# Performance work log

Measured on AMD Instinct MI355X. Metric: run time of the kernel, lower is better.

## Reference

```python
import jax, jax.numpy as jnp
import numpy as np

D = 768; NH = 12; HD = D // NH; L = 12; NC = 27; PATCH = 16; MLP = 3072; PROJ = 512
IMG = 224; GRID = IMG // PATCH; HW = GRID * GRID; S = NC + HW
NEG = -1e9

def _ln(x, w, b):
    m = jnp.mean(x, -1, keepdims=True)
    v = jnp.mean(jnp.square(x - m), -1, keepdims=True)
    return (x - m) * jax.lax.rsqrt(v + 1e-5) * w + b

def _quick_gelu(x):
    return x * jax.nn.sigmoid(1.702 * x)

def _build_mask(attn_obj_masks, dtype):
    # CRIS block mask: cls<->cls blocked except self; cls->patch allowed only for
    # patches of that class; patch->cls blocked; patch->patch fully allowed.
    B = attn_obj_masks.shape[0]
    oh = jax.nn.one_hot(attn_obj_masks, NC, dtype=dtype)              # [B, HW, NC]
    T11 = jnp.broadcast_to(1.0 - jnp.eye(NC, dtype=dtype), (B, NC, NC))
    M13 = 1.0 - jnp.swapaxes(oh, 1, 2)                                # [B, NC, HW]
    top = jnp.concatenate([T11, M13], axis=2)
    bot = jnp.concatenate([jnp.ones((B, HW, NC), dtype), jnp.zeros((B, HW, HW), dtype)], axis=2)
    Mb = jnp.concatenate([top, bot], axis=1)                          # [B, S, S]
    return jnp.where(Mb == 1.0, jnp.asarray(NEG, dtype), jnp.asarray(0.0, dtype))

def reference(img, sents, attn_obj_masks, obj_masks, cls_tokens, patch_w, patch_b, pos_embed,
              ln1_w, ln1_b, qkv_w, qkv_b, out_w, out_b, ln2_w, ln2_b,
              mlp_w1, mlp_b1, mlp_w2, mlp_b2, ln_post_w, ln_post_b, proj):
    B = img.shape[0]
    sents = sents / jnp.linalg.norm(sents, axis=-1, keepdims=True)    # encode_text output, L2 normed
    mask = _build_mask(attn_obj_masks, img.dtype)                     # [B, S, S]
    # patch embedding (conv stride 16) -> [B, HW, D]
    p = jax.lax.conv_general_dilated(img, patch_w, (PATCH, PATCH), 'VALID',
                                     dimension_numbers=('NCHW', 'OIHW', 'NCHW'))
    p = p.reshape(B, D, HW).transpose(0, 2, 1) + patch_b
    x = jnp.concatenate([jnp.broadcast_to(cls_tokens, (B, NC, D)), p], axis=1) + pos_embed
    scale = 1.0 / np.sqrt(HD).astype(np.float32)
    def block(x, prm):
        l1w, l1b, qw, qb, ow, ob, l2w, l2b, w1, b1, w2, b2 = prm
        h = _ln(x, l1w, l1b)
        qkv = h @ qw + qb
        q, k, v = jnp.split(qkv, 3, axis=-1)
        q = q.reshape(B, S, NH, HD).transpose(0, 2, 1, 3)
        k = k.reshape(B, S, NH, HD).transpose(0, 2, 1, 3)
        v = v.reshape(B, S, NH, HD).transpose(0, 2, 1, 3)
        scores = jnp.einsum('bhqd,bhkd->bhqk', q, k) * scale + mask[:, None]
        a = jax.nn.softmax(scores, axis=-1)
        o = jnp.einsum('bhqk,bhkd->bhqd', a, v).transpose(0, 2, 1, 3).reshape(B, S, D)
        x = x + o @ ow + ob
        h = _ln(x, l2w, l2b)
        x = x + _quick_gelu(h @ w1 + b1) @ w2 + b2
        return x, None
    x, _ = jax.lax.scan(block, x, (ln1_w, ln1_b, qkv_w, qkv_b, out_w, out_b,
                                   ln2_w, ln2_b, mlp_w1, mlp_b1, mlp_w2, mlp_b2))
    tokens = _ln(x, ln_post_w, ln_post_b) @ proj                      # [B, S, PROJ]
    obj = tokens[:, :NC]
    obj = obj / jnp.linalg.norm(obj, axis=-1, keepdims=True)
    pred_id = jnp.einsum('bnd,bd->bn', obj, sents)                    # [B, NC]
    # per-class scatter loop == gather of pred_id by per-pixel class id
    pred = jnp.take_along_axis(pred_id, obj_masks.reshape(B, -1), axis=1).reshape(obj_masks.shape)
    return pred                                                       # [B, 224, 224]

def setup_inputs():
    B = 16; std = 0.02
    ks = jax.random.split(jax.random.key(0), 16)
    f = jax.random.normal
    return {
        'img': f(ks[0], (B, 3, IMG, IMG), jnp.float32),
        'sents': f(ks[1], (B, PROJ), jnp.float32),
        'attn_obj_masks': jax.random.randint(ks[2], (B, HW), 0, NC, jnp.int32),
        'obj_masks': jax.random.randint(ks[3], (B, IMG, IMG), 0, NC, jnp.int32),
        'cls_tokens': f(ks[4], (1, NC, D)) * std,
        'patch_w': f(ks[5], (D, 3, PATCH, PATCH)) * std,
        'patch_b': jnp.zeros((D,)),
        'pos_embed': f(ks[6], (S, D)) * std,
        'ln1_w': jnp.ones((L, D)), 'ln1_b': jnp.zeros((L, D)),
        'qkv_w': f(ks[7], (L, D, 3 * D)) * std, 'qkv_b': jnp.zeros((L, 3 * D)),
        'out_w': f(ks[8], (L, D, D)) * std, 'out_b': jnp.zeros((L, D)),
        'ln2_w': jnp.ones((L, D)), 'ln2_b': jnp.zeros((L, D)),
        'mlp_w1': f(ks[9], (L, D, MLP)) * std, 'mlp_b1': jnp.zeros((L, MLP)),
        'mlp_w2': f(ks[10], (L, MLP, D)) * std, 'mlp_b2': jnp.zeros((L, D)),
        'ln_post_w': jnp.ones((D,)), 'ln_post_b': jnp.zeros((D,)),
        'proj': f(ks[11], (D, PROJ)) * std,
    }
```

## Files before the change

### kernel.cpp

```cpp
#include <hip/hip_runtime.h>

#define DEV __device__ __forceinline__

typedef short bf16x8 __attribute__((ext_vector_type(8)));
typedef float f32x4 __attribute__((ext_vector_type(4)));
typedef int vi4 __attribute__((ext_vector_type(4)));
typedef unsigned short u16;
typedef short short4v __attribute__((ext_vector_type(4)));

#define NEGV -1000000000.0f

DEV u16 f2bf(float f) {
  union { float f; unsigned u; } v; v.f = f;
  unsigned r = v.u + 0x7FFFu + ((v.u >> 16) & 1u);
  return (u16)(r >> 16);
}

DEV bf16x8 ld_bf8(const u16* p) {
  vi4 v = *(const vi4*)p;
  return __builtin_bit_cast(bf16x8, v);
}

DEV void gload_lds16(const u16* g, vi4* l) {
  __builtin_amdgcn_global_load_lds((const __attribute__((address_space(1))) void*)g,
                                   (__attribute__((address_space(3))) void*)l, 16, 0, 0);
}

template<int BN, int MODE, bool GELU, int KS>
__global__ __launch_bounds__(256) void gemm_bt(
    const u16* __restrict__ A, const u16* __restrict__ Bt,
    const float* __restrict__ bias,
    float* __restrict__ Cf, u16* __restrict__ Cb,
    int M, int N, int K, const float* __restrict__ pos, long pstride)
{
  constexpr int FJ = BN / 32;
  constexpr int LTOT = 4 + FJ;
  __shared__ vi4 As[2][1024];
  __shared__ vi4 Bs[2][BN * 8];

  int gx = gridDim.x, gy = gridDim.y;
  int nwg = gx * gy * (int)gridDim.z;
  int orig = blockIdx.x + gx * (blockIdx.y + gy * blockIdx.z);
  int qq = nwg >> 3, rr = nwg & 7;
  int xcd = orig & 7, off = orig >> 3;
  int id = (xcd < rr) ? xcd * (qq + 1) + off : rr * (qq + 1) + (xcd - rr) * qq + off;
  int bx = id % gx, rest = id / gx, by = rest % gy, bz = rest / gy;

  int tid = threadIdx.x, lane = tid & 63, wid = tid >> 6;
  int wm = wid >> 1, wn = wid & 1;
  int m0 = by * 128, n0 = bx * BN;
  int kBeg = (K / KS) * bz;
  int nT = (K / KS) >> 6;
  f32x4 acc[4][FJ] = {};

  auto STAGE = [&](int buf, int kk) {
    #pragma unroll
    for (int r = 0; r < 4; ++r) {
      int flat = r * 256 + tid;
      int row = flat >> 3, c = flat & 7;
      int cs = c ^ (row & 7);
      gload_lds16(A + (long)(m0 + row) * K + kk + cs * 8, &As[buf][r * 256 + wid * 64]);
    }
    #pragma unroll
    for (int r = 0; r < FJ; ++r) {
      int flat = r * 256 + tid;
      int row = flat >> 3, c = flat & 7;
      int cs = c ^ (row & 7);
      gload_lds16(Bt + (long)(n0 + row) * K + kk + cs * 8, &Bs[buf][r * 256 + wid * 64]);
    }
  };

  STAGE(0, kBeg);
  int cur = 0;
  for (int t = 0; t < nT; ++t) {
    if (t + 1 < nT) {
      STAGE(cur ^ 1, kBeg + (t + 1) * 64);
      asm volatile("s_waitcnt vmcnt(%0)" :: "i"(LTOT) : "memory");
    } else {
      asm volatile("s_waitcnt vmcnt(0)" ::: "memory");
    }
    __builtin_amdgcn_s_barrier();
    int cg = lane >> 4, l15 = lane & 15;
    #pragma unroll
    for (int ks = 0; ks < 2; ++ks) {
      bf16x8 af[4], bfr[FJ];
      #pragma unroll
      for (int i = 0; i < 4; ++i) {
        int ra = wm * 64 + i * 16 + l15;
        af[i] = __builtin_bit_cast(bf16x8, As[cur][ra * 8 + ((ks * 4 + cg) ^ (ra & 7))]);
      }
      #pragma unroll
      for (int j = 0; j < FJ; ++j) {
        int rb = wn * (BN / 2) + j * 16 + l15;
        bfr[j] = __builtin_bit_cast(bf16x8, Bs[cur][rb * 8 + ((ks * 4 + cg) ^ (rb & 7))]);
      }
      #pragma unroll
      for (int i = 0; i < 4; ++i)
        #pragma unroll
        for (int j = 0; j < FJ; ++j)
          acc[i][j] = __builtin_amdgcn_mfma_f32_16x16x32_bf16(af[i], bfr[j], acc[i][j], 0, 0, 0);
    }
    __builtin_amdgcn_s_barrier();
    cur ^= 1;
  }

  int cg = lane >> 4, l15 = lane & 15;
  float* Cfz = (MODE == 2 && KS > 1) ? Cf + (long)bz * pstride : Cf;
  #pragma unroll
  for (int i = 0; i < 4; ++i) {
    #pragma unroll
    for (int j = 0; j < FJ; ++j) {
      int col = n0 + wn * (BN / 2) + j * 16 + l15;
      float bv = bias ? bias[col] : 0.f;
      #pragma unroll
      for (int r = 0; r < 4; ++r) {
        int row = m0 + wm * 64 + i * 16 + cg * 4 + r;
        if (row < M) {
          float v = acc[i][j][r];
          if (KS == 1 || bz == 0) v += bv;
          if (GELU) v = v / (1.f + __expf(-1.702f * v));
          if (MODE == 0) Cb[(long)row * N + col] = f2bf(v);
          else if (MODE == 2) Cfz[(long)row * N + col] = v;
          else {
            int hw = row % 196;
            int xr = (row / 196) * 223 + 27 + hw;
            Cf[(long)xr * 768 + col] = v + pos[(27 + hw) * 768 + col];
          }
        }
      }
    }
  }
}

__global__ __launch_bounds__(256) void attn_kernel(
    const u16* __restrict__ QKV, const int* __restrict__ aom, u16* __restrict__ O)
{
  __shared__ vi4 Kl[224 * 8];
  __shared__ vi4 Vt[64 * 28];
  __shared__ vi4 Pl[4][16 * 28];
  __shared__ int ml[196];
  int tid = threadIdx.x, lane = tid & 63, wid = tid >> 6;
  int qg = blockIdx.x, h = blockIdx.y, b = blockIdx.z;
  long rowbase = (long)b * 223;
  #pragma unroll
  for (int it = 0; it < 7; ++it) {
    int flat = it * 256 + tid;
    int s = flat >> 3, c = flat & 7;
    int cs = c ^ (s & 7);
    gload_lds16(QKV + (rowbase + s) * 2304 + 768 + h * 64 + cs * 8, &Kl[it * 256 + wid * 64]);
  }
  u16* vt16 = (u16*)Vt;
  #pragma unroll
  for (int it = 0; it < 7; ++it) {
    int flat = it * 256 + tid;
    int s = flat >> 3, c = flat & 7;
    vi4 v = {0, 0, 0, 0};
    if (s < 223) v = *(const vi4*)(QKV + (rowbase + s) * 2304 + 1536 + h * 64 + c * 8);
    union { vi4 v4; u16 hx[8]; } uu; uu.v4 = v;
    int cs = s >> 3;
    #pragma unroll
    for (int j = 0; j < 8; ++j) {
      int d = c * 8 + j;
      vt16[d * 224 + (cs ^ ((d >> 1) & 3)) * 8 + (s & 7)] = uu.hx[j];
    }
  }
  for (int i = tid; i < 196; i += 256) ml[i] = aom[b * 196 + i];
  __syncthreads();

  int colk = lane & 15, cg = lane >> 4;
  #pragma unroll
  for (int rep = 0; rep < 2; ++rep) {
    int fo = wid * 2 + rep;
    if (fo >= 7) break;
    int qf = qg * 7 + fo;
    int q0 = qf * 16;
    int arow = q0 + colk; if (arow > 222) arow = 222;
    const u16* qb = QKV + (rowbase + arow) * 2304 + h * 64;
    bf16x8 aq0 = ld_bf8(qb + cg * 8);
    bf16x8 aq1 = ld_bf8(qb + 32 + cg * 8);

    f32x4 sc[14];
    #pragma unroll
    for (int kf = 0; kf < 14; ++kf) {
      int key = kf * 16 + colk;
      f32x4 a = {0.f, 0.f, 0.f, 0.f};
      bf16x8 bk0 = __builtin_bit_cast(bf16x8, Kl[key * 8 + (cg ^ (key & 7))]);
      bf16x8 bk1 = __builtin_bit_cast(bf16x8, Kl[key * 8 + ((4 + cg) ^ (key & 7))]);
      a = __builtin_amdgcn_mfma_f32_16x16x32_bf16(aq0, bk0, a, 0, 0, 0);
      a = __builtin_amdgcn_mfma_f32_16x16x32_bf16(aq1, bk1, a, 0, 0, 0);
      sc[kf] = a;
    }
    #pragma unroll
    for (int r = 0; r < 4; ++r) {
      int q = q0 + cg * 4 + r;
      float mx = -3.4e38f;
      #pragma unroll
      for (int kf = 0; kf < 14; ++kf) {
        int key = kf * 16 + colk;
        float mval;
        if (key >= 223) mval = NEGV;
        else if (q >= 27) mval = (key < 27) ? NEGV : 0.f;
        else if (key < 27) mval = (key == q) ? 0.f : NEGV;
        else mval = (ml[key - 27] == q) ? 0.f : NEGV;
        float s = sc[kf][r] * 0.125f + mval;
        sc[kf][r] = s;
        mx = fmaxf(mx, s);
      }
      #pragma unroll
      for (int d = 1; d < 16; d <<= 1) mx = fmaxf(mx, __shfl_xor(mx, d));
      float sum = 0.f;
      #pragma unroll
      for (int kf = 0; kf < 14; ++kf) {
        float e = __expf(sc[kf][r] - mx);
        sc[kf][r] = e; sum += e;
      }
      #pragma unroll
      for (int d = 1; d < 16; d <<= 1) sum += __shfl_xor(sum, d);
      float inv = 1.f / sum;
      #pragma unroll
      for (int kf = 0; kf < 14; ++kf) sc[kf][r] *= inv;
    }
    u16* pw = (u16*)Pl[wid];
    #pragma unroll
    for (int kf = 0; kf < 14; ++kf) {
      int key = kf * 16 + colk;
      int ck = key >> 3;
      #pragma unroll
      for (int r = 0; r < 4; ++r) {
        int prow = cg * 4 + r;
        pw[prow * 224 + (ck ^ ((prow >> 1) & 3)) * 8 + (key & 7)] = f2bf(sc[kf][r]);
      }
    }
    f32x4 oacc[4] = {};
    #pragma unroll
    for (int ks = 0; ks < 7; ++ks) {
      bf16x8 pa = __builtin_bit_cast(bf16x8, Pl[wid][colk * 28 + ((ks * 4 + cg) ^ ((colk >> 1) & 3))]);
      #pragma unroll
      for (int nf = 0; nf < 4; ++nf) {
        int d = nf * 16 + colk;
        bf16x8 bv = __builtin_bit_cast(bf16x8, Vt[d * 28 + ((ks * 4 + cg) ^ ((d >> 1) & 3))]);
        oacc[nf] = __builtin_amdgcn_mfma_f32_16x16x32_bf16(pa, bv, oacc[nf], 0, 0, 0);
      }
    }
    #pragma unroll
    for (int nf = 0; nf < 4; ++nf) {
      int d = h * 64 + nf * 16 + colk;
      #pragma unroll
      for (int r = 0; r < 4; ++r) {
        int q = q0 + cg * 4 + r;
        if (q < 223) O[(rowbase + q) * 768 + d] = f2bf(oacc[nf][r]);
      }
    }
  }
}

template<int NADD, bool MAP27, bool WRITEX>
__global__ __launch_bounds__(256) void ln_kernel(
    const float* __restrict__ X, const float* __restrict__ P, long ps,
    float* __restrict__ Xout, u16* __restrict__ Hb,
    const float* __restrict__ w, const float* __restrict__ bb, int nrows)
{
  int row = blockIdx.x * 4 + (threadIdx.x >> 6);
  if (row >= nrows) return;
  int xr = MAP27 ? (row / 27) * 223 + (row % 27) : row;
  int l = threadIdx.x & 63;
  const float4* xp = (const float4*)(X + (long)xr * 768);
  float4 a = xp[l], c = xp[l + 64], d = xp[l + 128];
  if (NADD == 2) {
    const float4* p0 = (const float4*)(P + (long)xr * 768);
    const float4* p1 = (const float4*)(P + ps + (long)xr * 768);
    float4 u0 = p0[l], u1 = p0[l + 64], u2 = p0[l + 128];
    float4 v0 = p1[l], v1 = p1[l + 64], v2 = p1[l + 128];
    a.x += u0.x + v0.x; a.y += u0.y + v0.y; a.z += u0.z + v0.z; a.w += u0.w + v0.w;
    c.x += u1.x + v1.x; c.y += u1.y + v1.y; c.z += u1.z + v1.z; c.w += u1.w + v1.w;
    d.x += u2.x + v2.x; d.y += u2.y + v2.y; d.z += u2.z + v2.z; d.w += u2.w + v2.w;
  }
  if (WRITEX) {
    float4* xo = (float4*)(Xout + (long)xr * 768);
    xo[l] = a; xo[l + 64] = c; xo[l + 128] = d;
  }
  float s = a.x + a.y + a.z + a.w + c.x + c.y + c.z + c.w + d.x + d.y + d.z + d.w;
  #pragma unroll
  for (int t = 1; t < 64; t <<= 1) s += __shfl_xor(s, t);
  float mean = s * (1.f / 768.f);
  a.x -= mean; a.y -= mean; a.z -= mean; a.w -= mean;
  c.x -= mean; c.y -= mean; c.z -= mean; c.w -= mean;
  d.x -= mean; d.y -= mean; d.z -= mean; d.w -= mean;
  float q = a.x*a.x + a.y*a.y + a.z*a.z + a.w*a.w
          + c.x*c.x + c.y*c.y + c.z*c.z + c.w*c.w
          + d.x*d.x + d.y*d.y + d.z*d.z + d.w*d.w;
  #pragma unroll
  for (int t = 1; t < 64; t <<= 1) q += __shfl_xor(q, t);
  float rs = rsqrtf(q * (1.f / 768.f) + 1e-5f);
  const float4* wp = (const float4*)w;
  const float4* bp = (const float4*)bb;
  u16* out = Hb + (long)row * 768;
  float4 w0 = wp[l], w1 = wp[l + 64], w2 = wp[l + 128];
  float4 b0 = bp[l], b1 = bp[l + 64], b2 = bp[l + 128];
  short4v o;
  o[0] = (short)f2bf(a.x * rs * w0.x + b0.x); o[1] = (short)f2bf(a.y * rs * w0.y + b0.y);
  o[2] = (short)f2bf(a.z * rs * w0.z + b0.z); o[3] = (short)f2bf(a.w * rs * w0.w + b0.w);
  *(short4v*)(out + l * 4) = o;
  o[0] = (short)f2bf(c.x * rs * w1.x + b1.x); o[1] = (short)f2bf(c.y * rs * w1.y + b1.y);
  o[2] = (short)f2bf(c.z * rs * w1.z + b1.z); o[3] = (short)f2bf(c.w * rs * w1.w + b1.w);
  *(short4v*)(out + 256 + l * 4) = o;
  o[0] = (short)f2bf(d.x * rs * w2.x + b2.x); o[1] = (short)f2bf(d.y * rs * w2.y + b2.y);
  o[2] = (short)f2bf(d.z * rs * w2.z + b2.z); o[3] = (short)f2bf(d.w * rs * w2.w + b2.w);
  *(short4v*)(out + 512 + l * 4) = o;
}

__global__ __launch_bounds__(256) void transpose_w(
    const float* __restrict__ W, u16* __restrict__ WT, int K, int N, long sW, long sT)
{
  __shared__ float t[64][65];
  int z = blockIdx.z;
  W += (long)z * sW; WT += (long)z * sT;
  int n0 = blockIdx.x * 64, k0 = blockIdx.y * 64;
  #pragma unroll
  for (int i = 0; i < 4; ++i) {
    int flat = i * 256 + threadIdx.x;
    int r = flat >> 4, c = (flat & 15) * 4;
    float4 v = *(const float4*)(W + (long)(k0 + r) * N + n0 + c);
    t[r][c] = v.x; t[r][c + 1] = v.y; t[r][c + 2] = v.z; t[r][c + 3] = v.w;
  }
  __syncthreads();
  #pragma unroll
  for (int i = 0; i < 8; ++i) {
    int flat = i * 256 + threadIdx.x;
    int rn = flat >> 5, ck = (flat & 31) * 2;
    unsigned val = (unsigned)f2bf(t[ck][rn]) | ((unsigned)f2bf(t[ck + 1][rn]) << 16);
    *(unsigned*)(WT + (long)(n0 + rn) * K + k0 + ck) = val;
  }
}

__global__ void convert_bf16(const float* __restrict__ src, u16* __restrict__ dst, int n) {
  int i = blockIdx.x * 256 + threadIdx.x;
  if (i < n) dst[i] = f2bf(src[i]);
}

__global__ __launch_bounds__(192) void patch_extract(const float* __restrict__ img, u16* __restrict__ Xp) {
  int row = blockIdx.x;
  int t = threadIdx.x;
  int pair = t >> 2, part = t & 3;
  int cch = pair >> 4, kh = pair & 15;
  int b = row / 196, hw = row % 196, gh = hw / 14, gw = hw % 14;
  float4 v = *(const float4*)(img + ((long)(b * 3 + cch) * 224 + gh * 16 + kh) * 224 + gw * 16 + part * 4);
  short4v o;
  o[0] = (short)f2bf(v.x); o[1] = (short)f2bf(v.y); o[2] = (short)f2bf(v.z); o[3] = (short)f2bf(v.w);
  *(short4v*)(Xp + (long)row * 768 + pair * 16 + part * 4) = o;
}

__global__ void cls_pos_fill(const float* __restrict__ cls, const float* __restrict__ pos, float* __restrict__ x) {
  int i = blockIdx.x * 256 + threadIdx.x;
  if (i >= 16 * 27 * 768) return;
  int d = i % 768, t = i / 768, b = t / 27, s = t % 27;
  x[((long)b * 223 + s) * 768 + d] = cls[s * 768 + d] + pos[s * 768 + d];
}

__global__ __launch_bounds__(256) void sents_norm(const float* __restrict__ s, float* __restrict__ sn) {
  __shared__ float sb[4];
  int b = blockIdx.x, t = threadIdx.x;
  float v0 = s[b * 512 + t], v1 = s[b * 512 + t + 256];
  float q = v0 * v0 + v1 * v1;
  #pragma unroll
  for (int d = 1; d < 64; d <<= 1) q += __shfl_xor(q, d);
  if ((t & 63) == 0) sb[t >> 6] = q;
  __syncthreads();
  float inv = rsqrtf(sb[0] + sb[1] + sb[2] + sb[3]);
  sn[b * 512 + t] = v0 * inv;
  sn[b * 512 + t + 256] = v1 * inv;
}

__global__ __launch_bounds__(256) void obj_dot(const float* __restrict__ obj, const float* __restrict__ sn, float* __restrict__ pid) {
  __shared__ float sb[8];
  int r = blockIdx.x, t = threadIdx.x, b = r / 27;
  float v0 = obj[(long)r * 512 + t], v1 = obj[(long)r * 512 + t + 256];
  float w0 = sn[b * 512 + t], w1 = sn[b * 512 + t + 256];
  float q = v0 * v0 + v1 * v1;
  float dt = v0 * w0 + v1 * w1;
  #pragma unroll
  for (int d = 1; d < 64; d <<= 1) { q += __shfl_xor(q, d); dt += __shfl_xor(dt, d); }
  if ((t & 63) == 0) { sb[t >> 6] = q; sb[4 + (t >> 6)] = dt; }
  __syncthreads();
  if (t == 0) pid[r] = (sb[4] + sb[5] + sb[6] + sb[7]) * rsqrtf(sb[0] + sb[1] + sb[2] + sb[3]);
}

__global__ void gather_pred(const int* __restrict__ om, const float* __restrict__ pid, float* __restrict__ out) {
  int i = blockIdx.x * 256 + threadIdx.x;
  if (i >= 16 * 224 * 224) return;
  int b = i / (224 * 224);
  out[i] = pid[b * 27 + om[i]];
}

extern "C" void kernel_launch(void* const* d_in, const int* in_sizes, int n_in,
                              void* d_out, int out_size, void* d_ws, size_t ws_size,
                              hipStream_t stream) {
  const float* img     = (const float*)d_in[0];
  const float* sents   = (const float*)d_in[1];
  const int*   aom     = (const int*)d_in[2];
  const int*   omask   = (const int*)d_in[3];
  const float* cls     = (const float*)d_in[4];
  const float* patch_w = (const float*)d_in[5];
  const float* patch_b = (const float*)d_in[6];
  const float* pos     = (const float*)d_in[7];
  const float* ln1w    = (const float*)d_in[8];
  const float* ln1b    = (const float*)d_in[9];
  const float* qkvw    = (const float*)d_in[10];
  const float* qkvb    = (const float*)d_in[11];
  const float* outw    = (const float*)d_in[12];
  const float* outb    = (const float*)d_in[13];
  const float* ln2w    = (const float*)d_in[14];
  const float* ln2b    = (const float*)d_in[15];
  const float* m1w     = (const float*)d_in[16];
  const float* m1b     = (const float*)d_in[17];
  const float* m2w     = (const float*)d_in[18];
  const float* m2b     = (const float*)d_in[19];
  const float* lnpw    = (const float*)d_in[20];
  const float* lnpb    = (const float*)d_in[21];
  const float* projw   = (const float*)d_in[22];

  char* p = (char*)d_ws;
  auto alloc = [&](size_t bytes) { char* r = p; p += (bytes + 255) & ~(size_t)255; return r; };
  const long PS = 3584l * 768;
  float* x   = (float*)alloc(3568ul * 768 * 4);
  u16* H     = (u16*)alloc(3584ul * 768 * 2);
  u16* QKV   = (u16*)alloc(3584ul * 2304 * 2);
  u16* Obuf  = (u16*)alloc(3584ul * 768 * 2);
  u16* G     = (u16*)alloc(3584ul * 3072 * 2);
  float* Y   = (float*)alloc((size_t)PS * 2 * 4);
  float* Mp  = (float*)alloc((size_t)PS * 2 * 4);
  u16* PWc   = (u16*)alloc(768ul * 768 * 2);
  u16* PrT   = (u16*)alloc(512ul * 768 * 2);
  float* obj = (float*)alloc(432ul * 512 * 4);
  float* sn  = (float*)alloc(16ul * 512 * 4);
  float* pid = (float*)alloc(432ul * 4);

  const size_t wlayer = (2304ul * 768 + 768ul * 768 + 3072ul * 768 + 768ul * 3072) * 2;
  size_t used = (size_t)(p - (char*)d_ws);
  int nw = (ws_size >= used + 12 * wlayer + 65536) ? 12 : 1;
  const long sQ = 2304l * 768, sO = 768l * 768, s1 = 768l * 3072, s2 = 3072l * 768;
  u16* WqT = (u16*)alloc((size_t)sQ * 2 * nw);
  u16* WoT = (u16*)alloc((size_t)sO * 2 * nw);
  u16* W1T = (u16*)alloc((size_t)s1 * 2 * nw);
  u16* W2T = (u16*)alloc((size_t)s2 * 2 * nw);

  convert_bf16<<<2304, 256, 0, stream>>>(patch_w, PWc, 768 * 768);
  transpose_w<<<dim3(8, 12, 1), 256, 0, stream>>>(projw, PrT, 768, 512, 0, 0);
  if (nw == 12) {
    transpose_w<<<dim3(36, 12, 12), 256, 0, stream>>>(qkvw, WqT, 768, 2304, sQ, sQ);
    transpose_w<<<dim3(12, 12, 12), 256, 0, stream>>>(outw, WoT, 768, 768, sO, sO);
    transpose_w<<<dim3(48, 12, 12), 256, 0, stream>>>(m1w, W1T, 768, 3072, s1, s1);
    transpose_w<<<dim3(12, 48, 12), 256, 0, stream>>>(m2w, W2T, 3072, 768, s2, s2);
  }
  patch_extract<<<3136, 192, 0, stream>>>(img, H);
  cls_pos_fill<<<1296, 256, 0, stream>>>(cls, pos, x);
  gemm_bt<64, 3, false, 1><<<dim3(12, 25), 256, 0, stream>>>(H, PWc, patch_b, x, nullptr, 3136, 768, 768, pos, 0);

  for (int l = 0; l < 12; ++l) {
    u16 *wq, *wo, *w1, *w2;
    if (nw == 12) { wq = WqT + (long)l * sQ; wo = WoT + (long)l * sO; w1 = W1T + (long)l * s1; w2 = W2T + (long)l * s2; }
    else {
      wq = WqT; wo = WoT; w1 = W1T; w2 = W2T;
      transpose_w<<<dim3(36, 12, 1), 256, 0, stream>>>(qkvw + (long)l * sQ, wq, 768, 2304, 0, 0);
      transpose_w<<<dim3(12, 12, 1), 256, 0, stream>>>(outw + (long)l * sO, wo, 768, 768, 0, 0);
      transpose_w<<<dim3(48, 12, 1), 256, 0, stream>>>(m1w + (long)l * s1, w1, 768, 3072, 0, 0);
      transpose_w<<<dim3(12, 48, 1), 256, 0, stream>>>(m2w + (long)l * s2, w2, 3072, 768, 0, 0);
    }
    if (l == 0)
      ln_kernel<0, false, false><<<892, 256, 0, stream>>>(x, nullptr, 0, nullptr, H, ln1w, ln1b, 3568);
    else
      ln_kernel<2, false, true><<<892, 256, 0, stream>>>(x, Mp, PS, x, H, ln1w + l * 768, ln1b + l * 768, 3568);
    gemm_bt<128, 0, false, 1><<<dim3(18, 28), 256, 0, stream>>>(H, wq, qkvb + l * 2304, nullptr, QKV, 3568, 2304, 768, nullptr, 0);
    attn_kernel<<<dim3(2, 12, 16), 256, 0, stream>>>(QKV, aom, Obuf);
    gemm_bt<64, 2, false, 2><<<dim3(12, 28, 2), 256, 0, stream>>>(Obuf, wo, outb + l * 768, Y, nullptr, 3568, 768, 768, nullptr, PS);
    ln_kernel<2, false, true><<<892, 256, 0, stream>>>(x, Y, PS, x, H, ln2w + l * 768, ln2b + l * 768, 3568);
    gemm_bt<128, 0, true, 1><<<dim3(24, 28), 256, 0, stream>>>(H, w1, m1b + l * 3072, nullptr, G, 3568, 3072, 768, nullptr, 0);
    gemm_bt<64, 2, false, 2><<<dim3(12, 28, 2), 256, 0, stream>>>(G, w2, m2b + l * 768, Mp, nullptr, 3568, 768, 3072, nullptr, PS);
  }

  ln_kernel<2, true, false><<<108, 256, 0, stream>>>(x, Mp, PS, nullptr, H, lnpw, lnpb, 432);
  gemm_bt<64, 2, false, 1><<<dim3(8, 4), 256, 0, stream>>>(H, PrT, nullptr, obj, nullptr, 432, 512, 768, nullptr, 0);
  sents_norm<<<16, 256, 0, stream>>>(sents, sn);
  obj_dot<<<432, 256, 0, stream>>>(obj, sn, pid);
  gather_pred<<<3136, 256, 0, stream>>>(omask, pid, (float*)d_out);
}
```

Measured before the change: 2.377 ms.

## Use transposed LDS reads for V and keep softmax probabilities in registers

The attention kernel now loads V directly into LDS with async global_load_lds in a swizzled row-major layout and reads it with ds_read_b64_tr_b16 transpose loads. This replaces the scalar per-element transpose scatter into LDS. It also swaps the QK^T MFMA operands so each lane holds one query's scores, which cuts the softmax reductions to two shuffles. Probabilities move between lanes by shuffles instead of a round trip through LDS. The cost is extra shuffles, an explicit lgkmcnt wait, and reliance on the gfx950 transpose-load instruction and its lane mapping being right.

```diff
diff --git a/kernel.cpp b/kernel.cpp
--- a/kernel.cpp
+++ b/kernel.cpp
@@ -5,6 +5,7 @@
 typedef short bf16x8 __attribute__((ext_vector_type(8)));
 typedef float f32x4 __attribute__((ext_vector_type(4)));
 typedef int vi4 __attribute__((ext_vector_type(4)));
+typedef unsigned uint2v __attribute__((ext_vector_type(2)));
 typedef unsigned short u16;
 typedef short short4v __attribute__((ext_vector_type(4)));
 
@@ -24,6 +25,16 @@
 DEV void gload_lds16(const u16* g, vi4* l) {
   __builtin_amdgcn_global_load_lds((const __attribute__((address_space(1))) void*)g,
                                    (__attribute__((address_space(3))) void*)l, 16, 0, 0);
+}
+
+DEV unsigned lds_off(const void* p) {
+  return (unsigned)(unsigned long long)(const __attribute__((address_space(3))) void*)p;
+}
+
+DEV uint2v ds_tr16(unsigned byteaddr) {
+  uint2v r;
+  asm volatile("ds_read_b64_tr_b16 %0, %1" : "=v"(r) : "v"(byteaddr));
+  return r;
 }
 
 template<int BN, int MODE, bool GELU, int KS>
@@ -136,8 +147,7 @@
     const u16* __restrict__ QKV, const int* __restrict__ aom, u16* __restrict__ O)
 {
   __shared__ vi4 Kl[224 * 8];
-  __shared__ vi4 Vt[64 * 28];
-  __shared__ vi4 Pl[4][16 * 28];
+  __shared__ vi4 Vl[224 * 8];
   __shared__ int ml[196];
   int tid = threadIdx.x, lane = tid & 63, wid = tid >> 6;
   int qg = blockIdx.x, h = blockIdx.y, b = blockIdx.z;
@@ -149,32 +159,27 @@
     int cs = c ^ (s & 7);
     gload_lds16(QKV + (rowbase + s) * 2304 + 768 + h * 64 + cs * 8, &Kl[it * 256 + wid * 64]);
   }
-  u16* vt16 = (u16*)Vt;
   #pragma unroll
   for (int it = 0; it < 7; ++it) {
-    int flat = it * 256 + tid;
-    int s = flat >> 3, c = flat & 7;
-    vi4 v = {0, 0, 0, 0};
-    if (s < 223) v = *(const vi4*)(QKV + (rowbase + s) * 2304 + 1536 + h * 64 + c * 8);
-    union { vi4 v4; u16 hx[8]; } uu; uu.v4 = v;
-    int cs = s >> 3;
-    #pragma unroll
-    for (int j = 0; j < 8; ++j) {
-      int d = c * 8 + j;
-      vt16[d * 224 + (cs ^ ((d >> 1) & 3)) * 8 + (s & 7)] = uu.hx[j];
-    }
+    int u = it * 256 + tid;
+    int slin = u >> 3, inner = u & 7;
+    int sk = slin >> 2, sdp = slin & 3;
+    int s = sk * 4 + (inner >> 1);
+    int c = ((sdp ^ (sk & 3)) << 1) | (inner & 1);
+    gload_lds16(QKV + (rowbase + s) * 2304 + 1536 + h * 64 + c * 8, &Vl[it * 256 + wid * 64]);
   }
   for (int i = tid; i < 196; i += 256) ml[i] = aom[b * 196 + i];
   __syncthreads();
 
-  int colk = lane & 15, cg = lane >> 4;
+  int l15 = lane & 15, cg = lane >> 4;
+  unsigned vbase = lds_off(Vl);
   #pragma unroll
   for (int rep = 0; rep < 2; ++rep) {
     int fo = wid * 2 + rep;
     if (fo >= 7) break;
     int qf = qg * 7 + fo;
     int q0 = qf * 16;
-    int arow = q0 + colk; if (arow > 222) arow = 222;
+    int arow = q0 + l15; if (arow > 222) arow = 222;
     const u16* qb = QKV + (rowbase + arow) * 2304 + h * 64;
     bf16x8 aq0 = ld_bf8(qb + cg * 8);
     bf16x8 aq1 = ld_bf8(qb + 32 + cg * 8);
@@ -182,73 +187,84 @@
     f32x4 sc[14];
     #pragma unroll
     for (int kf = 0; kf < 14; ++kf) {
-      int key = kf * 16 + colk;
+      int key = kf * 16 + l15;
       f32x4 a = {0.f, 0.f, 0.f, 0.f};
       bf16x8 bk0 = __builtin_bit_cast(bf16x8, Kl[key * 8 + (cg ^ (key & 7))]);
       bf16x8 bk1 = __builtin_bit_cast(bf16x8, Kl[key * 8 + ((4 + cg) ^ (key & 7))]);
-      a = __builtin_amdgcn_mfma_f32_16x16x32_bf16(aq0, bk0, a, 0, 0, 0);
-      a = __builtin_amdgcn_mfma_f32_16x16x32_bf16(aq1, bk1, a, 0, 0, 0);
+      a = __builtin_amdgcn_mfma_f32_16x16x32_bf16(bk0, aq0, a, 0, 0, 0);
+      a = __builtin_amdgcn_mfma_f32_16x16x32_bf16(bk1, aq1, a, 0, 0, 0);
       sc[kf] = a;
     }
-    #pragma unroll
-    for (int r = 0; r < 4; ++r) {
-      int q = q0 + cg * 4 + r;
-      float mx = -3.4e38f;
-      #pragma unroll
-      for (int kf = 0; kf < 14; ++kf) {
-        int key = kf * 16 + colk;
+    int q = q0 + l15;
+    float mx = -3.4e38f;
+    #pragma unroll
+    for (int kf = 0; kf < 14; ++kf) {
+      #pragma unroll
+      for (int r = 0; r < 4; ++r) {
+        int key = kf * 16 + cg * 4 + r;
         float mval;
         if (key >= 223) mval = NEGV;
         else if (q >= 27) mval = (key < 27) ? NEGV : 0.f;
         else if (key < 27) mval = (key == q) ? 0.f : NEGV;
         else mval = (ml[key - 27] == q) ? 0.f : NEGV;
-        float s = sc[kf][r] * 0.125f + mval;
-        sc[kf][r] = s;
-        mx = fmaxf(mx, s);
-      }
-      #pragma unroll
-      for (int d = 1; d < 16; d <<= 1) mx = fmaxf(mx, __shfl_xor(mx, d));
-      float sum = 0.f;
-      #pragma unroll
-      for (int kf = 0; kf < 14; ++kf) {
+        float sv = sc[kf][r] * 0.125f + mval;
+        sc[kf][r] = sv;
+        mx = fmaxf(mx, sv);
+      }
+    }
+    mx = fmaxf(mx, __shfl_xor(mx, 16));
+    mx = fmaxf(mx, __shfl_xor(mx, 32));
+    float sum = 0.f;
+    #pragma unroll
+    for (int kf = 0; kf < 14; ++kf) {
+      #pragma unroll
+      for (int r = 0; r < 4; ++r) {
         float e = __expf(sc[kf][r] - mx);
         sc[kf][r] = e; sum += e;
       }
-      #pragma unroll
-      for (int d = 1; d < 16; d <<= 1) sum += __shfl_xor(sum, d);
-      float inv = 1.f / sum;
-      #pragma unroll
-      for (int kf = 0; kf < 14; ++kf) sc[kf][r] *= inv;
-    }
-    u16* pw = (u16*)Pl[wid];
+    }
+    sum += __shfl_xor(sum, 16);
+    sum += __shfl_xor(sum, 32);
+    float inv = 1.f / sum;
+    unsigned plo[14], phi[14];
     #pragma unroll
     for (int kf = 0; kf < 14; ++kf) {
-      int key = kf * 16 + colk;
-      int ck = key >> 3;
+      plo[kf] = (unsigned)f2bf(sc[kf][0] * inv) | ((unsigned)f2bf(sc[kf][1] * inv) << 16);
+      phi[kf] = (unsigned)f2bf(sc[kf][2] * inv) | ((unsigned)f2bf(sc[kf][3] * inv) << 16);
+    }
+    f32x4 oacc[4] = {};
+    #pragma unroll
+    for (int ks = 0; ks < 7; ++ks) {
+      uint2v vr[4][2];
+      int sk0 = ks * 8 + cg * 2, sk1 = sk0 + 1;
+      #pragma unroll
+      for (int nf = 0; nf < 4; ++nf) {
+        vr[nf][0] = ds_tr16(vbase + (unsigned)(((sk0 * 4 + (nf ^ (sk0 & 3))) << 7) + l15 * 8));
+        vr[nf][1] = ds_tr16(vbase + (unsigned)(((sk1 * 4 + (nf ^ (sk1 & 3))) << 7) + l15 * 8));
+      }
+      int src0 = ((cg & 1) << 5) + l15, src1 = src0 + 16;
+      int lo0 = __shfl((int)plo[2 * ks], src0),     hi0 = __shfl((int)phi[2 * ks], src0);
+      int lo1 = __shfl((int)plo[2 * ks + 1], src0), hi1 = __shfl((int)phi[2 * ks + 1], src0);
+      int lo0b = __shfl((int)plo[2 * ks], src1),     hi0b = __shfl((int)phi[2 * ks], src1);
+      int lo1b = __shfl((int)plo[2 * ks + 1], src1), hi1b = __shfl((int)phi[2 * ks + 1], src1);
+      bool hg = (cg >> 1) & 1;
+      vi4 paw = { hg ? lo1 : lo0, hg ? hi1 : hi0, hg ? lo1b : lo0b, hg ? hi1b : hi0b };
+      bf16x8 pa = __builtin_bit_cast(bf16x8, paw);
+      asm volatile("s_waitcnt lgkmcnt(0)" ::: "memory");
+      __builtin_amdgcn_sched_barrier(0);
+      #pragma unroll
+      for (int nf = 0; nf < 4; ++nf) {
+        vi4 bw = { (int)vr[nf][0][0], (int)vr[nf][0][1], (int)vr[nf][1][0], (int)vr[nf][1][1] };
+        oacc[nf] = __builtin_amdgcn_mfma_f32_16x16x32_bf16(pa, __builtin_bit_cast(bf16x8, bw), oacc[nf], 0, 0, 0);
+      }
+    }
+    #pragma unroll
+    for (int nf = 0; nf < 4; ++nf) {
+      int d = h * 64 + nf * 16 + l15;
       #pragma unroll
       for (int r = 0; r < 4; ++r) {
-        int prow = cg * 4 + r;
-        pw[prow * 224 + (ck ^ ((prow >> 1) & 3)) * 8 + (key & 7)] = f2bf(sc[kf][r]);
-      }
-    }
-    f32x4 oacc[4] = {};
-    #pragma unroll
-    for (int ks = 0; ks < 7; ++ks) {
-      bf16x8 pa = __builtin_bit_cast(bf16x8, Pl[wid][colk * 28 + ((ks * 4 + cg) ^ ((colk >> 1) & 3))]);
-      #pragma unroll
-      for (int nf = 0; nf < 4; ++nf) {
-        int d = nf * 16 + colk;
-        bf16x8 bv = __builtin_bit_cast(bf16x8, Vt[d * 28 + ((ks * 4 + cg) ^ ((d >> 1) & 3))]);
-        oacc[nf] = __builtin_amdgcn_mfma_f32_16x16x32_bf16(pa, bv, oacc[nf], 0, 0, 0);
-      }
-    }
-    #pragma unroll
-    for (int nf = 0; nf < 4; ++nf) {
-      int d = h * 64 + nf * 16 + colk;
-      #pragma unroll
-      for (int r = 0; r < 4; ++r) {
-        int q = q0 + cg * 4 + r;
-        if (q < 223) O[(rowbase + q) * 768 + d] = f2bf(oacc[nf][r]);
+        int qo = q0 + cg * 4 + r;
+        if (qo < 223) O[(rowbase + qo) * 768 + d] = f2bf(oacc[nf][r]);
       }
     }
   }
```

Measured after the change: 2.150 ms. 1.11x faster.
